# Performance work log

Measured on AMD Instinct MI355X. Metric: run time of the kernel, lower is better.

## Reference

```python
import jax, jax.numpy as jnp
import numpy as np

BS, S, D, H = 4, 2048, 1024, 4096
TEMP, THRESH, PRIOR, EPS = 1.0, 0.5, 0.2, 1e-9


def setup_inputs() -> dict:
    key = jax.random.key(0)
    ks = jax.random.split(key, 4)
    hidden = jax.random.normal(ks[0], (BS, S, D), jnp.float32)
    # ragged valid lengths to exercise the padding / forced-last-boundary path
    lengths = jnp.array([S, S - 300, S - 700, S // 2], jnp.int32)
    attention_mask = (jnp.arange(S)[None, :] < lengths[:, None]).astype(jnp.float32)
    noise_u = jax.random.uniform(ks[1], (BS, S), jnp.float32, 1e-6, 1.0 - 1e-6)
    W1 = jax.random.normal(ks[2], (D, H), jnp.float32) * (1.0 / np.sqrt(D))
    b1 = jnp.zeros((H,), jnp.float32)
    W2 = jax.random.normal(ks[3], (H,), jnp.float32) * (1.0 / np.sqrt(H))
    b2 = jnp.zeros((), jnp.float32)
    return dict(hidden=hidden, attention_mask=attention_mask, noise_u=noise_u,
                W1=W1, b1=b1, W2=W2, b2=b2)


def reference(hidden, attention_mask, noise_u, W1, b1, W2, b2):
    bs, seq, _ = hidden.shape
    # tiny MLP gate -> per-token boundary logit
    h = jax.nn.relu(jnp.einsum('bsd,dh->bsh', hidden, W1) + b1)
    logits = jnp.einsum('bsh,h->bs', h, W2) + b2                     # [B,S]
    # RelaxedBernoulli(temp, probs=sigmoid(logits)).rsample()
    logistic = jnp.log(noise_u) - jnp.log1p(-noise_u)
    soft = jax.nn.sigmoid((logits + logistic) / TEMP)
    # straight-through hard boundaries
    hard = (soft > THRESH).astype(soft.dtype)
    hard = jax.lax.stop_gradient(hard - soft) + soft
    # mask out padding, force a boundary on the last real token of each row
    hard = hard * attention_mask
    pad = attention_mask == 0
    first_pad = pad & (jnp.cumsum(pad.astype(jnp.int32), axis=1) == 1)
    last_real = jnp.roll(first_pad, shift=-1, axis=1)
    last_real = last_real.at[:, -1].set(False)
    hard = jnp.maximum(hard, last_real.astype(hard.dtype))
    # downsample: mean-pool tokens within segments ending at boundary tokens
    hh1 = jnp.cumsum(hard, axis=1) - hard                            # [B,S] segment id of each token
    foo = jnp.arange(seq, dtype=hard.dtype)[None, None, :] - hh1[:, :, None]  # [B,S_tok,S_seg]
    lel = jnp.where(foo == 0, 1.0 - foo, 0.0)                        # one-hot (diff. via -foo)
    bar = lel / (jnp.sum(lel, axis=1, keepdims=True) + EPS)          # normalize per segment
    pooled = jnp.einsum('bld,bls->bsd', hidden, bar)                 # [B,S_seg,D] (zero-padded beyond max #segments)
    # binomial boundary-rate loss
    num_b = jnp.sum(hard)
    total = jnp.sum(attention_mask)
    gln = jax.scipy.special.gammaln
    log_prob = (gln(total + 1.0) - gln(num_b + 1.0) - gln(total - num_b + 1.0)
                + num_b * jnp.log(PRIOR) + (total - num_b) * jnp.log(1.0 - PRIOR))
    loss = -log_prob / total
    # shortened attention mask: kept positions all have mask==1, so it is a
    # left-packed ones mask of length = #boundaries per row (zero-padded to S)
    counts = jnp.sum(jax.lax.stop_gradient(hard), axis=1)
    short_mask = (jnp.arange(seq, dtype=counts.dtype)[None, :] < counts[:, None]).astype(jnp.float32)
    return pooled, loss, num_b, total, short_mask
```

## Files before the change

kernel.cpp:

```cpp
#include <hip/hip_runtime.h>
#include <math.h>

#define BSZ 4
#define SEQ 2048
#define DIM 1024
#define HID 4096
#define MTOT (BSZ * SEQ)
#define NHB 64
#define EPSF 1e-9f

#define BM 256
#define BN 256
#define BKF 32
#define KITERS (DIM / BKF)
#define BSCALE 32.0f
#define INV_BSCALE (1.0f / 32.0f)

typedef _Float16 f16;
typedef _Float16 f16x4 __attribute__((ext_vector_type(4)));
typedef _Float16 f16x8 __attribute__((ext_vector_type(8)));
typedef float f32x16 __attribute__((ext_vector_type(16)));

__device__ __forceinline__ void gl16(const f16* g, f16* l) {
  __builtin_amdgcn_global_load_lds(
      (const __attribute__((address_space(1))) void*)g,
      (__attribute__((address_space(3))) void*)l, 16, 0, 0);
}

__global__ void split_a(const float* __restrict__ in, f16* __restrict__ hi,
                        f16* __restrict__ lo) {
  int i = blockIdx.x * 256 + threadIdx.x;
  float4 v = ((const float4*)in)[i];
  f16x4 h, l;
  h.x = (f16)v.x; h.y = (f16)v.y; h.z = (f16)v.z; h.w = (f16)v.w;
  l.x = (f16)(v.x - (float)h.x);
  l.y = (f16)(v.y - (float)h.y);
  l.z = (f16)(v.z - (float)h.z);
  l.w = (f16)(v.w - (float)h.w);
  ((f16x4*)hi)[i] = h;
  ((f16x4*)lo)[i] = l;
}

__global__ void split_w1t(const float* __restrict__ w1, f16* __restrict__ hi,
                          f16* __restrict__ lo) {
  __shared__ float tile[32][36];
  const int k0 = blockIdx.x * 32;
  const int h0 = blockIdx.y * 32;
  const int t = threadIdx.x;
  {
    int kk = t >> 3, hq = (t & 7) * 4;
    float4 v = *(const float4*)&w1[(size_t)(k0 + kk) * HID + h0 + hq];
    tile[kk][hq + 0] = v.x; tile[kk][hq + 1] = v.y;
    tile[kk][hq + 2] = v.z; tile[kk][hq + 3] = v.w;
  }
  __syncthreads();
  int hh = t >> 3, kq = (t & 7) * 4;
  f16x4 H, L;
#pragma unroll
  for (int j = 0; j < 4; ++j) {
    float x = tile[kq + j][hh] * BSCALE;
    f16 xh = (f16)x;
    H[j] = xh;
    L[j] = (f16)(x - (float)xh);
  }
  *(f16x4*)&hi[(size_t)(h0 + hh) * DIM + k0 + kq] = H;
  *(f16x4*)&lo[(size_t)(h0 + hh) * DIM + k0 + kq] = L;
}

__global__ __launch_bounds__(512, 2)
void gate_gemm(const f16* __restrict__ Ahi, const f16* __restrict__ Alo,
               const f16* __restrict__ Whi, const f16* __restrict__ Wlo,
               const float* __restrict__ b1, const float* __restrict__ W2,
               float* __restrict__ partial) {
  __shared__ f16 sA[2][BM][64];
  __shared__ f16 sB[2][BN][64];

  const int bid = blockIdx.x;
  const int wg = (bid & 7) * 64 + (bid >> 3);
  const int nt = wg >> 5;
  const int mt = wg & 31;
  const int m0 = mt * BM, h0 = nt * BN;

  const int t = threadIdx.x;
  const int lane = t & 63, wid = t >> 6;
  const int wm = wid >> 2, wn = wid & 3;
  const int rowl = lane & 31, kb = lane >> 5;
  const int sl0 = kb, sl1 = 2 + kb;

  f32x16 acc[4][2];
#pragma unroll
  for (int a = 0; a < 4; ++a)
#pragma unroll
    for (int b = 0; b < 2; ++b)
#pragma unroll
      for (int e = 0; e < 16; ++e) acc[a][b][e] = 0.f;

  const f16* srcA[4];
  const f16* srcB[4];
#pragma unroll
  for (int i = 0; i < 4; ++i) {
    int sig = i * 512 + t;
    int r = sig >> 3, p = sig & 7;
    int q = p ^ (r & 7);
    int koff = (q & 3) * 8;
    srcA[i] = (q < 4 ? Ahi : Alo) + (size_t)(m0 + r) * DIM + koff;
    srcB[i] = (q < 4 ? Whi : Wlo) + (size_t)(h0 + r) * DIM + koff;
  }

#define STAGE_B2(buf_, kt_, j)                                                \
  { _Pragma("unroll") for (int i = 2 * (j); i < 2 * (j) + 2; ++i) {           \
      gl16(srcB[i] + (size_t)(kt_) * BKF,                                     \
           &sB[buf_][0][0] + (i * 512 + wid * 64) * 8);                       \
  } }
#define STAGE_A2(buf_, kt_, j)                                                \
  { _Pragma("unroll") for (int ii = 0; ii < 2; ++ii) {                        \
      int i = (j) + ii * 2;                                                   \
      gl16(srcA[i] + (size_t)(kt_) * BKF,                                     \
           &sA[buf_][0][0] + (i * 512 + wid * 64) * 8);                       \
  } }

#define LDA2(fmb, sl)                                                         \
  { _Pragma("unroll") for (int f = 0; f < 2; ++f) {                           \
      int ra = wm * 128 + ((fmb) + f) * 32 + rowl;                            \
      int ph = ((sl) ^ (ra & 7)) * 8;                                         \
      ah[f] = *(const f16x8*)&sA[buf][ra][ph];                                \
      al[f] = *(const f16x8*)&sA[buf][ra][ph ^ 32];                           \
  } }
#define LDB2(sl)                                                              \
  { _Pragma("unroll") for (int n = 0; n < 2; ++n) {                           \
      int rb = wn * 64 + n * 32 + rowl;                                       \
      int pb = ((sl) ^ (rb & 7)) * 8;                                         \
      bh[n] = *(const f16x8*)&sB[buf][rb][pb];                                \
      bl[n] = *(const f16x8*)&sB[buf][rb][pb ^ 32];                           \
  } }

#define MFMA12(fmb)                                                           \
  { _Pragma("unroll") for (int f = 0; f < 2; ++f)                             \
      _Pragma("unroll") for (int n = 0; n < 2; ++n)                           \
        acc[(fmb) + f][n] = __builtin_amdgcn_mfma_f32_32x32x16_f16(           \
            ah[f], bh[n], acc[(fmb) + f][n], 0, 0, 0);                        \
    _Pragma("unroll") for (int f = 0; f < 2; ++f)                             \
      _Pragma("unroll") for (int n = 0; n < 2; ++n)                           \
        acc[(fmb) + f][n] = __builtin_amdgcn_mfma_f32_32x32x16_f16(           \
            ah[f], bl[n], acc[(fmb) + f][n], 0, 0, 0);                        \
    _Pragma("unroll") for (int f = 0; f < 2; ++f)                             \
      _Pragma("unroll") for (int n = 0; n < 2; ++n)                           \
        acc[(fmb) + f][n] = __builtin_amdgcn_mfma_f32_32x32x16_f16(           \
            al[f], bh[n], acc[(fmb) + f][n], 0, 0, 0); }

#define SBAR                                                                  \
  { __builtin_amdgcn_sched_barrier(0); __builtin_amdgcn_s_barrier();          \
    __builtin_amdgcn_sched_barrier(0); }
#define LGKM0                                                                 \
  { asm volatile("s_waitcnt lgkmcnt(0)" ::: "memory");                        \
    __builtin_amdgcn_sched_barrier(0); }

  STAGE_B2(0, 0, 0); STAGE_B2(0, 0, 1);
  STAGE_A2(0, 0, 0); STAGE_A2(0, 0, 1);
  asm volatile("s_waitcnt vmcnt(2)" ::: "memory");
  SBAR;

  for (int kt = 0; kt < KITERS; ++kt) {
    const int buf = kt & 1;
    const int nbuf = buf ^ 1;
    const bool notlast = (kt + 1 < KITERS);
    f16x8 ah[2], al[2], bh[2], bl[2];

    LDA2(0, sl0); LDB2(sl0);
    if (notlast) STAGE_B2(nbuf, kt + 1, 0);
    SBAR;
    LGKM0;
    __builtin_amdgcn_s_setprio(1);
    MFMA12(0);
    __builtin_amdgcn_s_setprio(0);
    __builtin_amdgcn_sched_barrier(0);
    if (notlast) { asm volatile("s_waitcnt vmcnt(2)" ::: "memory"); }
    else         { asm volatile("s_waitcnt vmcnt(0)" ::: "memory"); }
    SBAR;

    LDA2(2, sl0);
    if (notlast) STAGE_B2(nbuf, kt + 1, 1);
    SBAR;
    LGKM0;
    __builtin_amdgcn_s_setprio(1);
    MFMA12(2);
    __builtin_amdgcn_s_setprio(0);
    SBAR;

    LDA2(0, sl1); LDB2(sl1);
    if (notlast) STAGE_A2(nbuf, kt + 1, 0);
    SBAR;
    LGKM0;
    __builtin_amdgcn_s_setprio(1);
    MFMA12(0);
    __builtin_amdgcn_s_setprio(0);
    SBAR;

    LDA2(2, sl1);
    if (notlast) STAGE_A2(nbuf, kt + 1, 1);
    SBAR;
    LGKM0;
    __builtin_amdgcn_s_setprio(1);
    MFMA12(2);
    __builtin_amdgcn_s_setprio(0);
    __builtin_amdgcn_sched_barrier(0);
    if (notlast) { asm volatile("s_waitcnt vmcnt(2)" ::: "memory"); }
    SBAR;
  }

  float b1v[2], w2v[2];
#pragma unroll
  for (int fn = 0; fn < 2; ++fn) {
    int h = h0 + wn * 64 + fn * 32 + rowl;
    b1v[fn] = b1[h];
    w2v[fn] = W2[h];
  }
#pragma unroll
  for (int fm = 0; fm < 4; ++fm)
#pragma unroll
    for (int r = 0; r < 16; ++r) {
      float v0 = acc[fm][0][r] * INV_BSCALE + b1v[0];
      float v1 = acc[fm][1][r] * INV_BSCALE + b1v[1];
      acc[fm][0][r] = fmaxf(v0, 0.f) * w2v[0] + fmaxf(v1, 0.f) * w2v[1];
    }
#pragma unroll
  for (int off = 1; off <= 16; off <<= 1)
#pragma unroll
    for (int fm = 0; fm < 4; ++fm)
#pragma unroll
      for (int r = 0; r < 16; ++r)
        acc[fm][0][r] += __shfl_xor(acc[fm][0][r], off);
  if (rowl == 0) {
    const int hb = nt * 4 + wn;
#pragma unroll
    for (int fm = 0; fm < 4; ++fm)
#pragma unroll
      for (int r = 0; r < 16; ++r) {
        int token = m0 + wm * 128 + fm * 32 + (r & 3) + 8 * (r >> 2) + 4 * kb;
        partial[(size_t)hb * MTOT + token] = acc[fm][0][r];
      }
  }
}

__global__ void reduce_logits(const float* __restrict__ partial,
                              float* __restrict__ logits) {
  int s = blockIdx.x * 256 + threadIdx.x;
  float lg = 0.f;
#pragma unroll
  for (int h = 0; h < NHB; ++h) lg += partial[(size_t)h * MTOT + s];
  logits[s] = lg;
}

__global__ void boundary_scan(const float* __restrict__ logits,
                              const float* __restrict__ mask,
                              const float* __restrict__ noise,
                              const float* __restrict__ b2,
                              int* __restrict__ bpos, int* __restrict__ counts,
                              int* __restrict__ lengths,
                              float* __restrict__ shortmask) {
  const int b = blockIdx.x;
  const int t = threadIdx.x;
  __shared__ float hardS[SEQ];
  __shared__ float red[256];
  const float bias2 = b2[0];

  float msum = 0.f;
  for (int s = t; s < SEQ; s += 256) {
    float lg = logits[b * SEQ + s] + bias2;
    float u = noise[b * SEQ + s];
    float lgt = logf(u) - log1pf(-u);
    float m = mask[b * SEQ + s];
    float hard = ((lg + lgt) > 0.f) ? 1.f : 0.f;
    hardS[s] = hard * m;
    msum += m;
  }
  red[t] = msum;
  __syncthreads();
  for (int off = 128; off > 0; off >>= 1) {
    if (t < off) red[t] += red[t + off];
    __syncthreads();
  }
  int L = (int)(red[0] + 0.5f);
  __syncthreads();
  if (t == 0) {
    if (L < SEQ) hardS[L - 1] = fmaxf(hardS[L - 1], 1.f);
    lengths[b] = L;
  }
  __syncthreads();

  float loc[8];
  float run = 0.f;
#pragma unroll
  for (int i = 0; i < 8; ++i) { loc[i] = hardS[t * 8 + i]; run += loc[i]; }
  red[t] = run;
  __syncthreads();
  for (int off = 1; off < 256; off <<= 1) {
    float v = (t >= off) ? red[t - off] : 0.f;
    __syncthreads();
    red[t] += v;
    __syncthreads();
  }
  float base = red[t] - run;
  int cnt = (int)(red[255] + 0.5f);

  float pre = base;
#pragma unroll
  for (int i = 0; i < 8; ++i) {
    if (loc[i] > 0.5f) {
      int rank = (int)(pre + 0.5f);
      bpos[b * SEQ + rank] = t * 8 + i;
    }
    pre += loc[i];
  }
  if (t == 0) counts[b] = cnt;
  for (int s = t; s < SEQ; s += 256)
    shortmask[b * SEQ + s] = (s < cnt) ? 1.f : 0.f;
}

__global__ void pool_seg(const float* __restrict__ hidden,
                         const int* __restrict__ bpos,
                         const int* __restrict__ counts,
                         float* __restrict__ pooled) {
  const int g = blockIdx.x, b = blockIdx.y;
  const int t = threadIdx.x;
  const int cnt = counts[b];
  float4 acc = {0.f, 0.f, 0.f, 0.f};
  float* outp = pooled + ((size_t)(b * SEQ + g)) * DIM + t * 4;
  if (g > cnt) { *(float4*)outp = acc; return; }
  if (g == cnt) return;
  int start = (g == 0) ? 0 : bpos[b * SEQ + g - 1] + 1;
  int end = bpos[b * SEQ + g] + 1;
  const float* hb = hidden + ((size_t)b * SEQ) * DIM + t * 4;
  for (int l = start; l < end; ++l) {
    float4 v = *(const float4*)(hb + (size_t)l * DIM);
    acc.x += v.x; acc.y += v.y; acc.z += v.z; acc.w += v.w;
  }
  float inv = 1.f / ((float)(end - start) + EPSF);
  acc.x *= inv; acc.y *= inv; acc.z *= inv; acc.w *= inv;
  *(float4*)outp = acc;
}

__global__ void pool_tail_partial(const float* __restrict__ hidden,
                                  const int* __restrict__ bpos,
                                  const int* __restrict__ counts,
                                  float* __restrict__ tailpart) {
  const int c = blockIdx.x;
  const int b = blockIdx.y;
  const int t = threadIdx.x;
  int cnt = counts[b];
  int start = (cnt == 0) ? 0 : bpos[b * SEQ + cnt - 1] + 1;
  int n = SEQ - start;
  int clen = (n + 15) / 16;
  int s0 = start + c * clen;
  int s1 = s0 + clen; if (s1 > SEQ) s1 = SEQ;
  float4 acc = {0.f, 0.f, 0.f, 0.f};
  const float* hb = hidden + ((size_t)b * SEQ) * DIM + t * 4;
  for (int l = s0; l < s1; ++l) {
    float4 v = *(const float4*)(hb + (size_t)l * DIM);
    acc.x += v.x; acc.y += v.y; acc.z += v.z; acc.w += v.w;
  }
  *(float4*)(tailpart + ((size_t)(b * 16 + c)) * DIM + t * 4) = acc;
}

__global__ void pool_tail_final(const int* __restrict__ bpos,
                                const int* __restrict__ counts,
                                const float* __restrict__ tailpart,
                                float* __restrict__ pooled) {
  const int b = blockIdx.x;
  const int t = threadIdx.x;
  int cnt = counts[b];
  if (cnt >= SEQ) return;
  int start = (cnt == 0) ? 0 : bpos[b * SEQ + cnt - 1] + 1;
  float4 acc = {0.f, 0.f, 0.f, 0.f};
  for (int c = 0; c < 16; ++c) {
    float4 v = *(const float4*)(tailpart + ((size_t)(b * 16 + c)) * DIM + t * 4);
    acc.x += v.x; acc.y += v.y; acc.z += v.z; acc.w += v.w;
  }
  float inv = 1.f / ((float)(SEQ - start) + EPSF);
  acc.x *= inv; acc.y *= inv; acc.z *= inv; acc.w *= inv;
  *(float4*)(pooled + ((size_t)(b * SEQ + cnt)) * DIM + t * 4) = acc;
}

__global__ void loss_kernel(const int* __restrict__ counts,
                            const int* __restrict__ lengths,
                            float* __restrict__ outScalars) {
  if (threadIdx.x != 0 || blockIdx.x != 0) return;
  double num_b = 0.0, total = 0.0;
  for (int b = 0; b < BSZ; ++b) { num_b += (double)counts[b]; total += (double)lengths[b]; }
  double lp = lgamma(total + 1.0) - lgamma(num_b + 1.0) - lgamma(total - num_b + 1.0)
            + num_b * log(0.2) + (total - num_b) * log(0.8);
  outScalars[0] = (float)(-lp / total);
  outScalars[1] = (float)num_b;
  outScalars[2] = (float)total;
}

extern "C" void kernel_launch(void* const* d_in, const int* in_sizes, int n_in,
                              void* d_out, int out_size, void* d_ws, size_t ws_size,
                              hipStream_t stream) {
  const float* hidden = (const float*)d_in[0];
  const float* mask   = (const float*)d_in[1];
  const float* noise  = (const float*)d_in[2];
  const float* W1     = (const float*)d_in[3];
  const float* b1     = (const float*)d_in[4];
  const float* W2     = (const float*)d_in[5];
  const float* b2     = (const float*)d_in[6];

  float* out = (float*)d_out;
  float* pooled = out;
  float* scalars = out + (size_t)BSZ * SEQ * DIM;
  float* shortmask = scalars + 3;

  char* ws = (char*)d_ws;
  size_t off = 0;
  float* partial = (float*)(ws + off); off += (size_t)NHB * MTOT * sizeof(float);
  f16* Ahi = (f16*)(ws + off); off += (size_t)MTOT * DIM * sizeof(f16);
  f16* Alo = (f16*)(ws + off); off += (size_t)MTOT * DIM * sizeof(f16);
  f16* Whi = (f16*)(ws + off); off += (size_t)HID * DIM * sizeof(f16);
  f16* Wlo = (f16*)(ws + off); off += (size_t)HID * DIM * sizeof(f16);
  float* logits = (float*)(ws + off); off += (size_t)MTOT * sizeof(float);
  int* bpos = (int*)(ws + off); off += (size_t)BSZ * SEQ * sizeof(int);
  int* counts = (int*)(ws + off); off += 16 * sizeof(int);
  int* lengths = (int*)(ws + off); off += 16 * sizeof(int);
  off = (off + 255) & ~(size_t)255;
  float* tailpart = (float*)(ws + off);

  split_a<<<MTOT * DIM / 4 / 256, 256, 0, stream>>>(hidden, Ahi, Alo);
  split_w1t<<<dim3(DIM / 32, HID / 32), 256, 0, stream>>>(W1, Whi, Wlo);
  gate_gemm<<<(MTOT / BM) * (HID / BN), 512, 0, stream>>>(Ahi, Alo, Whi, Wlo,
                                                          b1, W2, partial);
  reduce_logits<<<MTOT / 256, 256, 0, stream>>>(partial, logits);
  boundary_scan<<<BSZ, 256, 0, stream>>>(logits, mask, noise, b2,
                                         bpos, counts, lengths, shortmask);
  pool_tail_partial<<<dim3(16, BSZ), 256, 0, stream>>>(hidden, bpos, counts, tailpart);
  pool_seg<<<dim3(SEQ, BSZ), 256, 0, stream>>>(hidden, bpos, counts, pooled);
  pool_tail_final<<<BSZ, 256, 0, stream>>>(bpos, counts, tailpart, pooled);
  loss_kernel<<<1, 1, 0, stream>>>(counts, lengths, scalars);
}
```

Baseline: 269.5 us.

## Fuse split kernels, make GEMM persistent over two M-tiles, fold logit reduction into scan

Merges the activation and weight fp16 split kernels into a single launch. The gate GEMM now launches one block per CU, each processing two M-tiles sequentially in one continuous pipelined K loop with an epilogue between tiles. The separate logit reduction kernel is removed and its 64-way partial sum is done inside the boundary scan. This cuts launches and tile tail effects but moves the reduction into a 4-block kernel with low parallelism.

```diff
diff --git a/kernel.cpp b/kernel.cpp
--- a/kernel.cpp
+++ b/kernel.cpp
@@ -27,26 +27,31 @@
       (__attribute__((address_space(3))) void*)l, 16, 0, 0);
 }
 
-__global__ void split_a(const float* __restrict__ in, f16* __restrict__ hi,
-                        f16* __restrict__ lo) {
-  int i = blockIdx.x * 256 + threadIdx.x;
-  float4 v = ((const float4*)in)[i];
-  f16x4 h, l;
-  h.x = (f16)v.x; h.y = (f16)v.y; h.z = (f16)v.z; h.w = (f16)v.w;
-  l.x = (f16)(v.x - (float)h.x);
-  l.y = (f16)(v.y - (float)h.y);
-  l.z = (f16)(v.z - (float)h.z);
-  l.w = (f16)(v.w - (float)h.w);
-  ((f16x4*)hi)[i] = h;
-  ((f16x4*)lo)[i] = l;
-}
-
-__global__ void split_w1t(const float* __restrict__ w1, f16* __restrict__ hi,
-                          f16* __restrict__ lo) {
+#define NA_BLOCKS (MTOT * DIM / 4 / 256)
+#define NW_BLOCKS ((DIM / 32) * (HID / 32))
+
+__global__ void split_all(const float* __restrict__ inA, f16* __restrict__ Ahi,
+                          f16* __restrict__ Alo, const float* __restrict__ w1,
+                          f16* __restrict__ Whi, f16* __restrict__ Wlo) {
   __shared__ float tile[32][36];
-  const int k0 = blockIdx.x * 32;
-  const int h0 = blockIdx.y * 32;
-  const int t = threadIdx.x;
+  const int bid = blockIdx.x;
+  const int t = threadIdx.x;
+  if (bid < NA_BLOCKS) {
+    int i = bid * 256 + t;
+    float4 v = ((const float4*)inA)[i];
+    f16x4 h, l;
+    h.x = (f16)v.x; h.y = (f16)v.y; h.z = (f16)v.z; h.w = (f16)v.w;
+    l.x = (f16)(v.x - (float)h.x);
+    l.y = (f16)(v.y - (float)h.y);
+    l.z = (f16)(v.z - (float)h.z);
+    l.w = (f16)(v.w - (float)h.w);
+    ((f16x4*)Ahi)[i] = h;
+    ((f16x4*)Alo)[i] = l;
+    return;
+  }
+  const int wb = bid - NA_BLOCKS;
+  const int k0 = (wb & 31) * 32;
+  const int h0 = (wb >> 5) * 32;
   {
     int kk = t >> 3, hq = (t & 7) * 4;
     float4 v = *(const float4*)&w1[(size_t)(k0 + kk) * HID + h0 + hq];
@@ -63,9 +68,11 @@
     H[j] = xh;
     L[j] = (f16)(x - (float)xh);
   }
-  *(f16x4*)&hi[(size_t)(h0 + hh) * DIM + k0 + kq] = H;
-  *(f16x4*)&lo[(size_t)(h0 + hh) * DIM + k0 + kq] = L;
-}
+  *(f16x4*)&Whi[(size_t)(h0 + hh) * DIM + k0 + kq] = H;
+  *(f16x4*)&Wlo[(size_t)(h0 + hh) * DIM + k0 + kq] = L;
+}
+
+#define A2OFF ((size_t)16 * BM * DIM)
 
 __global__ __launch_bounds__(512, 2)
 void gate_gemm(const f16* __restrict__ Ahi, const f16* __restrict__ Alo,
@@ -76,9 +83,9 @@
   __shared__ f16 sB[2][BN][64];
 
   const int bid = blockIdx.x;
-  const int wg = (bid & 7) * 64 + (bid >> 3);
-  const int nt = wg >> 5;
-  const int mt = wg & 31;
+  const int wg = (bid & 7) * 32 + (bid >> 3);
+  const int nt = wg >> 4;
+  const int mt = wg & 15;
   const int m0 = mt * BM, h0 = nt * BN;
 
   const int t = threadIdx.x;
@@ -109,13 +116,13 @@
 
 #define STAGE_B2(buf_, kt_, j)                                                \
   { _Pragma("unroll") for (int i = 2 * (j); i < 2 * (j) + 2; ++i) {           \
-      gl16(srcB[i] + (size_t)(kt_) * BKF,                                     \
+      gl16(srcB[i] + (size_t)((kt_) & 31) * BKF,                              \
            &sB[buf_][0][0] + (i * 512 + wid * 64) * 8);                       \
   } }
 #define STAGE_A2(buf_, kt_, j)                                                \
   { _Pragma("unroll") for (int ii = 0; ii < 2; ++ii) {                        \
       int i = (j) + ii * 2;                                                   \
-      gl16(srcA[i] + (size_t)(kt_) * BKF,                                     \
+      gl16(srcA[i] + (size_t)((kt_) & 31) * BKF + ((kt_) >> 5) * A2OFF,       \
            &sA[buf_][0][0] + (i * 512 + wid * 64) * 8);                       \
   } }
 
@@ -155,15 +162,48 @@
   { asm volatile("s_waitcnt lgkmcnt(0)" ::: "memory");                        \
     __builtin_amdgcn_sched_barrier(0); }
 
+#define EPILOG(tile_)                                                         \
+  {                                                                           \
+    float b1v[2], w2v[2];                                                     \
+    _Pragma("unroll") for (int fn = 0; fn < 2; ++fn) {                        \
+      int h = h0 + wn * 64 + fn * 32 + rowl;                                  \
+      b1v[fn] = b1[h];                                                        \
+      w2v[fn] = W2[h];                                                        \
+    }                                                                         \
+    _Pragma("unroll") for (int fm = 0; fm < 4; ++fm)                          \
+      _Pragma("unroll") for (int r = 0; r < 16; ++r) {                        \
+        float v0 = acc[fm][0][r] * INV_BSCALE + b1v[0];                       \
+        float v1 = acc[fm][1][r] * INV_BSCALE + b1v[1];                       \
+        acc[fm][0][r] = fmaxf(v0, 0.f) * w2v[0] + fmaxf(v1, 0.f) * w2v[1];    \
+      }                                                                       \
+    _Pragma("unroll") for (int off = 1; off <= 16; off <<= 1)                 \
+      _Pragma("unroll") for (int fm = 0; fm < 4; ++fm)                        \
+        _Pragma("unroll") for (int r = 0; r < 16; ++r)                        \
+          acc[fm][0][r] += __shfl_xor(acc[fm][0][r], off);                    \
+    if (rowl == 0) {                                                          \
+      const int hb = nt * 4 + wn;                                             \
+      _Pragma("unroll") for (int fm = 0; fm < 4; ++fm)                        \
+        _Pragma("unroll") for (int r = 0; r < 16; ++r) {                      \
+          int token = m0 + (tile_) * 4096 + wm * 128 + fm * 32 +              \
+                      (r & 3) + 8 * (r >> 2) + 4 * kb;                        \
+          partial[(size_t)hb * MTOT + token] = acc[fm][0][r];                 \
+        }                                                                     \
+    }                                                                         \
+    _Pragma("unroll") for (int a = 0; a < 4; ++a)                             \
+      _Pragma("unroll") for (int b = 0; b < 2; ++b)                           \
+        _Pragma("unroll") for (int e = 0; e < 16; ++e) acc[a][b][e] = 0.f;    \
+  }
+
   STAGE_B2(0, 0, 0); STAGE_B2(0, 0, 1);
   STAGE_A2(0, 0, 0); STAGE_A2(0, 0, 1);
   asm volatile("s_waitcnt vmcnt(2)" ::: "memory");
   SBAR;
 
-  for (int kt = 0; kt < KITERS; ++kt) {
+#pragma unroll 1
+  for (int kt = 0; kt < 2 * KITERS; ++kt) {
     const int buf = kt & 1;
     const int nbuf = buf ^ 1;
-    const bool notlast = (kt + 1 < KITERS);
+    const bool notlast = (kt + 1 < 2 * KITERS);
     f16x8 ah[2], al[2], bh[2], bl[2];
 
     LDA2(0, sl0); LDB2(sl0);
@@ -206,52 +246,13 @@
     __builtin_amdgcn_sched_barrier(0);
     if (notlast) { asm volatile("s_waitcnt vmcnt(2)" ::: "memory"); }
     SBAR;
-  }
-
-  float b1v[2], w2v[2];
-#pragma unroll
-  for (int fn = 0; fn < 2; ++fn) {
-    int h = h0 + wn * 64 + fn * 32 + rowl;
-    b1v[fn] = b1[h];
-    w2v[fn] = W2[h];
-  }
-#pragma unroll
-  for (int fm = 0; fm < 4; ++fm)
-#pragma unroll
-    for (int r = 0; r < 16; ++r) {
-      float v0 = acc[fm][0][r] * INV_BSCALE + b1v[0];
-      float v1 = acc[fm][1][r] * INV_BSCALE + b1v[1];
-      acc[fm][0][r] = fmaxf(v0, 0.f) * w2v[0] + fmaxf(v1, 0.f) * w2v[1];
-    }
-#pragma unroll
-  for (int off = 1; off <= 16; off <<= 1)
-#pragma unroll
-    for (int fm = 0; fm < 4; ++fm)
-#pragma unroll
-      for (int r = 0; r < 16; ++r)
-        acc[fm][0][r] += __shfl_xor(acc[fm][0][r], off);
-  if (rowl == 0) {
-    const int hb = nt * 4 + wn;
-#pragma unroll
-    for (int fm = 0; fm < 4; ++fm)
-#pragma unroll
-      for (int r = 0; r < 16; ++r) {
-        int token = m0 + wm * 128 + fm * 32 + (r & 3) + 8 * (r >> 2) + 4 * kb;
-        partial[(size_t)hb * MTOT + token] = acc[fm][0][r];
-      }
-  }
-}
-
-__global__ void reduce_logits(const float* __restrict__ partial,
-                              float* __restrict__ logits) {
-  int s = blockIdx.x * 256 + threadIdx.x;
-  float lg = 0.f;
-#pragma unroll
-  for (int h = 0; h < NHB; ++h) lg += partial[(size_t)h * MTOT + s];
-  logits[s] = lg;
-}
-
-__global__ void boundary_scan(const float* __restrict__ logits,
+
+    if (kt == KITERS - 1) EPILOG(0);
+  }
+  EPILOG(1);
+}
+
+__global__ void boundary_scan(const float* __restrict__ partial,
                               const float* __restrict__ mask,
                               const float* __restrict__ noise,
                               const float* __restrict__ b2,
@@ -266,7 +267,9 @@
 
   float msum = 0.f;
   for (int s = t; s < SEQ; s += 256) {
-    float lg = logits[b * SEQ + s] + bias2;
+    float lg = bias2;
+#pragma unroll
+    for (int h = 0; h < NHB; ++h) lg += partial[(size_t)h * MTOT + b * SEQ + s];
     float u = noise[b * SEQ + s];
     float lgt = logf(u) - log1pf(-u);
     float m = mask[b * SEQ + s];
@@ -417,19 +420,16 @@
   f16* Alo = (f16*)(ws + off); off += (size_t)MTOT * DIM * sizeof(f16);
   f16* Whi = (f16*)(ws + off); off += (size_t)HID * DIM * sizeof(f16);
   f16* Wlo = (f16*)(ws + off); off += (size_t)HID * DIM * sizeof(f16);
-  float* logits = (float*)(ws + off); off += (size_t)MTOT * sizeof(float);
   int* bpos = (int*)(ws + off); off += (size_t)BSZ * SEQ * sizeof(int);
   int* counts = (int*)(ws + off); off += 16 * sizeof(int);
   int* lengths = (int*)(ws + off); off += 16 * sizeof(int);
   off = (off + 255) & ~(size_t)255;
   float* tailpart = (float*)(ws + off);
 
-  split_a<<<MTOT * DIM / 4 / 256, 256, 0, stream>>>(hidden, Ahi, Alo);
-  split_w1t<<<dim3(DIM / 32, HID / 32), 256, 0, stream>>>(W1, Whi, Wlo);
-  gate_gemm<<<(MTOT / BM) * (HID / BN), 512, 0, stream>>>(Ahi, Alo, Whi, Wlo,
-                                                          b1, W2, partial);
-  reduce_logits<<<MTOT / 256, 256, 0, stream>>>(partial, logits);
-  boundary_scan<<<BSZ, 256, 0, stream>>>(logits, mask, noise, b2,
+  split_all<<<NA_BLOCKS + NW_BLOCKS, 256, 0, stream>>>(hidden, Ahi, Alo,
+                                                       W1, Whi, Wlo);
+  gate_gemm<<<256, 512, 0, stream>>>(Ahi, Alo, Whi, Wlo, b1, W2, partial);
+  boundary_scan<<<BSZ, 256, 0, stream>>>(partial, mask, noise, b2,
                                          bpos, counts, lengths, shortmask);
   pool_tail_partial<<<dim3(16, BSZ), 256, 0, stream>>>(hidden, bpos, counts, tailpart);
   pool_seg<<<dim3(SEQ, BSZ), 256, 0, stream>>>(hidden, bpos, counts, pooled);
```

Result: faster. 254.2 us (-5.7%).
